# Kernel optimization log

Measured on AMD Instinct MI355X. Metric: run time of the kernel, lower is better.

## Reference

```python
import jax, jax.numpy as jnp
import numpy as np

# torch_dtype_to_gain is an undefined global in the original source; we interpret
# it as the standard sqrt(d_k) attention gain for the input dtype.

def reference(qk, qk_scaling_factor, query, key, value):
    D = query.shape[-1]
    gain = jnp.sqrt(jnp.asarray(D, dtype=query.dtype))
    # scores: [B, Sq, Sk]
    scores = jnp.einsum('bqd,bkd->bqk', query, key)
    scores = scores / gain
    scores = scores / qk_scaling_factor  # broadcast [1,1]
    # p=0.0, is_training=False -> dropout is identity
    o = jnp.einsum('bqk,bkv->bqv', scores, value)  # [B, Sq, Dv]
    return o


def setup_inputs() -> dict:
    key0 = jax.random.key(0)
    k1, k2, k3, k4 = jax.random.split(key0, 4)
    B, Sq, Sk, D, Dv = 8, 2048, 2048, 128, 128
    return {
        'qk': jnp.ones((1, 1), dtype=jnp.float32),  # overwritten in forward; dummy
        'qk_scaling_factor': jnp.ones((1, 1), dtype=jnp.float32),
        'query': jax.random.normal(k1, (B, Sq, D), dtype=jnp.float32),
        'key': jax.random.normal(k2, (B, Sk, D), dtype=jnp.float32),
        'value': jax.random.normal(k3, (B, Sk, Dv), dtype=jnp.float32),
    }
```

## Files before the change

### kernel.cpp

```cpp
#include <hip/hip_runtime.h>


#define BATCH 8
#define SEQ 2048
#define DIM 128

typedef __attribute__((ext_vector_type(8))) short short8;
typedef __attribute__((ext_vector_type(4))) float f32x4;

__device__ __forceinline__ unsigned int f2bf(float f) {
    unsigned int u = __float_as_uint(f);
    u += 0x7fffu + ((u >> 16) & 1u);
    return u >> 16;
}

__global__ __launch_bounds__(256) void vtk_partial(const float* __restrict__ K,
                                                   const float* __restrict__ V,
                                                   unsigned short* __restrict__ P) {
    __shared__ float Vc[64 * 128];
    __shared__ float Kc[64 * 64];
    const int blk = blockIdx.x;
    const int b   = blk >> 6;
    const int kc  = (blk >> 1) & 31;
    const int dh  = blk & 1;
    const int tid = threadIdx.x;

    const float* Vg = V + ((size_t)b * SEQ + kc * 64) * DIM;
    const float* Kg = K + ((size_t)b * SEQ + kc * 64) * DIM + dh * 64;

    #pragma unroll
    for (int i = 0; i < 8; i++) {
        int idx = tid + i * 256;
        ((float4*)Vc)[idx] = ((const float4*)Vg)[idx];
    }
    #pragma unroll
    for (int i = 0; i < 4; i++) {
        int idx = tid + i * 256;
        int r = idx >> 4, c = idx & 15;
        ((float4*)Kc)[idx] = *(const float4*)(Kg + r * DIM + c * 4);
    }
    __syncthreads();

    const int td = tid & 15;
    const int te = tid >> 4;

    float acc[8][4];
    #pragma unroll
    for (int i = 0; i < 8; i++)
        #pragma unroll
        for (int j = 0; j < 4; j++) acc[i][j] = 0.0f;

    for (int k = 0; k < 64; k++) {
        const float4 kd = *(const float4*)&Kc[k * 64 + td * 4];
        const float4 va = *(const float4*)&Vc[k * 128 + te * 8];
        const float4 vb = *(const float4*)&Vc[k * 128 + te * 8 + 4];
        const float ve[8] = {va.x, va.y, va.z, va.w, vb.x, vb.y, vb.z, vb.w};
        const float kv[4] = {kd.x, kd.y, kd.z, kd.w};
        #pragma unroll
        for (int i = 0; i < 8; i++)
            #pragma unroll
            for (int j = 0; j < 4; j++)
                acc[i][j] = fmaf(ve[i], kv[j], acc[i][j]);
    }

    unsigned short* Pb = P + (size_t)blk * 8192;
    #pragma unroll
    for (int i = 0; i < 8; i++) {
        uint2 w;
        w.x = f2bf(acc[i][0]) | (f2bf(acc[i][1]) << 16);
        w.y = f2bf(acc[i][2]) | (f2bf(acc[i][3]) << 16);
        *(uint2*)(Pb + (te * 8 + i) * 64 + td * 4) = w;
    }
}

__global__ __launch_bounds__(256) void reduce_t(const unsigned short* __restrict__ P,
                                                const float* __restrict__ qk_sf,
                                                unsigned short* __restrict__ Tt) {
    const int u   = blockIdx.x * 256 + threadIdx.x;
    const int b   = u >> 12;
    const int rem = u & 4095;
    const int e   = rem >> 5;
    const int d0  = (rem & 31) * 4;
    const int dh  = d0 >> 6;
    const int dl  = d0 & 63;

    const unsigned short* Pb = P + ((size_t)(b * 64 + dh) * 8192) + e * 64 + dl;
    float a0 = 0.f, a1 = 0.f, a2 = 0.f, a3 = 0.f;
    #pragma unroll 8
    for (int kc = 0; kc < 32; kc++) {
        uint2 w = *(const uint2*)(Pb + (size_t)kc * 16384);
        a0 += __uint_as_float(w.x << 16);
        a1 += __uint_as_float(w.x & 0xffff0000u);
        a2 += __uint_as_float(w.y << 16);
        a3 += __uint_as_float(w.y & 0xffff0000u);
    }
    const float s = 1.0f / (sqrtf(128.0f) * qk_sf[0]);
    uint2 o;
    o.x = f2bf(a0 * s) | (f2bf(a1 * s) << 16);
    o.y = f2bf(a2 * s) | (f2bf(a3 * s) << 16);
    *(uint2*)(Tt + (size_t)b * 16384 + e * 128 + d0) = o;
}

__global__ __launch_bounds__(256) void qt_mfma(const float* __restrict__ Q,
                                               const unsigned short* __restrict__ Tt,
                                               float* __restrict__ O) {
    __shared__ unsigned short Ts[128 * 136];
    __shared__ unsigned short Qs[32 * 136];
    const int b   = blockIdx.x >> 6;
    const int q0  = (blockIdx.x & 63) * 32;
    const int tid = threadIdx.x;

    const uint4* Tg = (const uint4*)(Tt + (size_t)b * 16384);
    #pragma unroll
    for (int i = 0; i < 8; i++) {
        int idx = tid + i * 256;
        int row = idx >> 4, c = idx & 15;
        *(uint4*)&Ts[row * 136 + c * 8] = Tg[idx];
    }
    const float4* Qg = (const float4*)(Q + ((size_t)b * SEQ + q0) * DIM);
    #pragma unroll
    for (int i = 0; i < 4; i++) {
        int idx = tid + i * 256;
        int row = idx >> 5, c = idx & 31;
        float4 v = Qg[idx];
        uint2 w;
        w.x = f2bf(v.x) | (f2bf(v.y) << 16);
        w.y = f2bf(v.z) | (f2bf(v.w) << 16);
        *(uint2*)&Qs[row * 136 + c * 4] = w;
    }
    __syncthreads();

    const int wave = tid >> 6, lane = tid & 63;
    const int lm   = lane & 15, quad = lane >> 4;
    const int mrow = (wave & 1) * 16;
    const int n0   = (wave >> 1) * 64;

    f32x4 acc[4] = {{0,0,0,0},{0,0,0,0},{0,0,0,0},{0,0,0,0}};
    #pragma unroll
    for (int ks = 0; ks < 4; ks++) {
        short8 a = *(const short8*)&Qs[(mrow + lm) * 136 + ks * 32 + quad * 8];
        #pragma unroll
        for (int nt = 0; nt < 4; nt++) {
            short8 bb = *(const short8*)&Ts[(n0 + nt * 16 + lm) * 136 + ks * 32 + quad * 8];
            acc[nt] = __builtin_amdgcn_mfma_f32_16x16x32_bf16(a, bb, acc[nt], 0, 0, 0);
        }
    }

    float* Og = O + ((size_t)b * SEQ + q0) * DIM;
    #pragma unroll
    for (int nt = 0; nt < 4; nt++)
        #pragma unroll
        for (int r = 0; r < 4; r++) {
            const int row = mrow + quad * 4 + r;
            const int col = n0 + nt * 16 + lm;
            Og[row * DIM + col] = acc[nt][r];
        }
}

extern "C" void kernel_launch(void* const* d_in, const int* in_sizes, int n_in,
                              void* d_out, int out_size, void* d_ws, size_t ws_size,
                              hipStream_t stream) {
    const float* qk_sf = (const float*)d_in[1];
    const float* Q = (const float*)d_in[2];
    const float* K = (const float*)d_in[3];
    const float* V = (const float*)d_in[4];
    float* O = (float*)d_out;

    unsigned short* P  = (unsigned short*)d_ws;
    unsigned short* Tt = (unsigned short*)((char*)d_ws + (size_t)512 * 8192 * 2);

    vtk_partial<<<dim3(512), dim3(256), 0, stream>>>(K, V, P);
    reduce_t<<<dim3(128), dim3(256), 0, stream>>>(P, qk_sf, Tt);
    qt_mfma<<<dim3(BATCH * 64), dim3(256), 0, stream>>>(Q, Tt, O);
}
```

Baseline: 96.54 us.

## Retile V^T K partials to full 128x128 per 32-key chunk with 8x8 register tiles

The V^T·K partial kernel now has each block cover a 32-key chunk across the full 128x128 output, using 8x8 per-thread register tiles instead of a 64-key chunk split over two D halves with 8x4 tiles. This drops the duplicate V loads across the D split and raises FMA-per-LDS-load reuse. In exchange the partial buffer doubles, since there are 64 chunks per batch instead of 32, so the reduction kernel must read twice as many bf16 partials. The reduction is rewritten to use more threads that each handle two elements, with narrower loads.

```diff
diff --git a/kernel.cpp b/kernel.cpp
--- a/kernel.cpp
+++ b/kernel.cpp
@@ -17,59 +17,57 @@
 __global__ __launch_bounds__(256) void vtk_partial(const float* __restrict__ K,
                                                    const float* __restrict__ V,
                                                    unsigned short* __restrict__ P) {
-    __shared__ float Vc[64 * 128];
-    __shared__ float Kc[64 * 64];
+    __shared__ float Kc[32 * 128];
+    __shared__ float Vc[32 * 128];
     const int blk = blockIdx.x;
     const int b   = blk >> 6;
-    const int kc  = (blk >> 1) & 31;
-    const int dh  = blk & 1;
+    const int kc  = blk & 63;
     const int tid = threadIdx.x;
 
-    const float* Vg = V + ((size_t)b * SEQ + kc * 64) * DIM;
-    const float* Kg = K + ((size_t)b * SEQ + kc * 64) * DIM + dh * 64;
-
-    #pragma unroll
-    for (int i = 0; i < 8; i++) {
-        int idx = tid + i * 256;
-        ((float4*)Vc)[idx] = ((const float4*)Vg)[idx];
-    }
+    const float4* Kg = (const float4*)(K + ((size_t)b * SEQ + kc * 32) * DIM);
+    const float4* Vg = (const float4*)(V + ((size_t)b * SEQ + kc * 32) * DIM);
     #pragma unroll
     for (int i = 0; i < 4; i++) {
         int idx = tid + i * 256;
-        int r = idx >> 4, c = idx & 15;
-        ((float4*)Kc)[idx] = *(const float4*)(Kg + r * DIM + c * 4);
+        ((float4*)Kc)[idx] = Kg[idx];
+        ((float4*)Vc)[idx] = Vg[idx];
     }
     __syncthreads();
 
     const int td = tid & 15;
     const int te = tid >> 4;
 
-    float acc[8][4];
+    float acc[8][8];
     #pragma unroll
     for (int i = 0; i < 8; i++)
         #pragma unroll
-        for (int j = 0; j < 4; j++) acc[i][j] = 0.0f;
+        for (int j = 0; j < 8; j++) acc[i][j] = 0.0f;
 
-    for (int k = 0; k < 64; k++) {
-        const float4 kd = *(const float4*)&Kc[k * 64 + td * 4];
-        const float4 va = *(const float4*)&Vc[k * 128 + te * 8];
-        const float4 vb = *(const float4*)&Vc[k * 128 + te * 8 + 4];
-        const float ve[8] = {va.x, va.y, va.z, va.w, vb.x, vb.y, vb.z, vb.w};
-        const float kv[4] = {kd.x, kd.y, kd.z, kd.w};
+    #pragma unroll 4
+    for (int k = 0; k < 32; k++) {
+        const float4 k0 = *(const float4*)&Kc[k * 128 + td * 8];
+        const float4 k1 = *(const float4*)&Kc[k * 128 + td * 8 + 4];
+        const float4 v0 = *(const float4*)&Vc[k * 128 + te * 8];
+        const float4 v1 = *(const float4*)&Vc[k * 128 + te * 8 + 4];
+        const float kd[8] = {k0.x, k0.y, k0.z, k0.w, k1.x, k1.y, k1.z, k1.w};
+        const float ve[8] = {v0.x, v0.y, v0.z, v0.w, v1.x, v1.y, v1.z, v1.w};
         #pragma unroll
         for (int i = 0; i < 8; i++)
             #pragma unroll
-            for (int j = 0; j < 4; j++)
-                acc[i][j] = fmaf(ve[i], kv[j], acc[i][j]);
+            for (int j = 0; j < 8; j++)
+                acc[i][j] = fmaf(ve[i], kd[j], acc[i][j]);
     }
 
-    unsigned short* Pb = P + (size_t)blk * 8192;
+    unsigned short* Pb = P + (size_t)blk * 16384;
     #pragma unroll
     for (int i = 0; i < 8; i++) {
-        uint2 w;
+        const int e = te * 8 + i;
+        uint4 w;
         w.x = f2bf(acc[i][0]) | (f2bf(acc[i][1]) << 16);
         w.y = f2bf(acc[i][2]) | (f2bf(acc[i][3]) << 16);
-        *(uint2*)(Pb + (te * 8 + i) * 64 + td * 4) = w;
+        w.z = f2bf(acc[i][4]) | (f2bf(acc[i][5]) << 16);
+        w.w = f2bf(acc[i][6]) | (f2bf(acc[i][7]) << 16);
+        *(uint4*)(Pb + e * 128 + td * 8) = w;
     }
 }
 
@@ -77,28 +75,20 @@
                                                 const float* __restrict__ qk_sf,
                                                 unsigned short* __restrict__ Tt) {
     const int u   = blockIdx.x * 256 + threadIdx.x;
-    const int b   = u >> 12;
-    const int rem = u & 4095;
-    const int e   = rem >> 5;
-    const int d0  = (rem & 31) * 4;
-    const int dh  = d0 >> 6;
-    const int dl  = d0 & 63;
+    const int b   = u >> 13;
+    const int rem = u & 8191;
 
-    const unsigned short* Pb = P + ((size_t)(b * 64 + dh) * 8192) + e * 64 + dl;
-    float a0 = 0.f, a1 = 0.f, a2 = 0.f, a3 = 0.f;
+    const unsigned short* Pb = P + (size_t)b * 64 * 16384 + rem * 2;
+    float a0 = 0.f, a1 = 0.f;
     #pragma unroll 8
-    for (int kc = 0; kc < 32; kc++) {
-        uint2 w = *(const uint2*)(Pb + (size_t)kc * 16384);
-        a0 += __uint_as_float(w.x << 16);
-        a1 += __uint_as_float(w.x & 0xffff0000u);
-        a2 += __uint_as_float(w.y << 16);
-        a3 += __uint_as_float(w.y & 0xffff0000u);
+    for (int kc = 0; kc < 64; kc++) {
+        unsigned int w = *(const unsigned int*)(Pb + (size_t)kc * 16384);
+        a0 += __uint_as_float(w << 16);
+        a1 += __uint_as_float(w & 0xffff0000u);
     }
     const float s = 1.0f / (sqrtf(128.0f) * qk_sf[0]);
-    uint2 o;
-    o.x = f2bf(a0 * s) | (f2bf(a1 * s) << 16);
-    o.y = f2bf(a2 * s) | (f2bf(a3 * s) << 16);
-    *(uint2*)(Tt + (size_t)b * 16384 + e * 128 + d0) = o;
+    unsigned int o = f2bf(a0 * s) | (f2bf(a1 * s) << 16);
+    *(unsigned int*)(Tt + (size_t)b * 16384 + rem * 2) = o;
 }
 
 __global__ __launch_bounds__(256) void qt_mfma(const float* __restrict__ Q,
@@ -167,9 +157,9 @@
     float* O = (float*)d_out;
 
     unsigned short* P  = (unsigned short*)d_ws;
-    unsigned short* Tt = (unsigned short*)((char*)d_ws + (size_t)512 * 8192 * 2);
+    unsigned short* Tt = (unsigned short*)((char*)d_ws + (size_t)512 * 16384 * 2);
 
     vtk_partial<<<dim3(512), dim3(256), 0, stream>>>(K, V, P);
-    reduce_t<<<dim3(128), dim3(256), 0, stream>>>(P, qk_sf, Tt);
+    reduce_t<<<dim3(256), dim3(256), 0, stream>>>(P, qk_sf, Tt);
     qt_mfma<<<dim3(BATCH * 64), dim3(256), 0, stream>>>(Q, Tt, O);
 }
```

After: 99.87 us. 3.5% more time.
